# Performance work log

Hardware: AMD Instinct MI355X
Metric: run time of the kernel (lower is better)

## Reference

```python
import jax, jax.numpy as jnp
import numpy as np

GAMMA = 2.0

def setup_inputs() -> dict:
    key = jax.random.key(0)
    k1, k2, k3, k4 = jax.random.split(key, 4)
    B, N, D, C = 4, 512, 128, 10
    x = jax.random.normal(k1, (B, N, D), dtype=jnp.float32)
    span = jax.random.randint(k2, (B, N, N), 0, C, dtype=jnp.int32)
    seqlen = jax.random.randint(k3, (B,), 1, N + 1, dtype=jnp.int32)
    W = jax.random.truncated_normal(k4, -2.0, 2.0, (D, C), dtype=jnp.float32) * 0.02
    b = jnp.zeros((C,), dtype=jnp.float32)
    return {"x": x, "span": span, "seqlen": seqlen, "W": W, "b": b}

def reference(x, span, seqlen, W, b):
    B, N, D = x.shape
    # pairwise tile-multiply: xx[b,i,j,d] = x[b,i,d] * x[b,j,d]
    xx = x[:, :, None, :] * x[:, None, :, :]            # [B,N,N,D]
    logits = jnp.einsum('bijd,dc->bijc', xx, W) + b     # [B,N,N,C]
    sm = jax.nn.softmax(logits, axis=-1)
    # focal loss: gather prob of true class
    prob = jnp.take_along_axis(sm, span[..., None].astype(jnp.int32), axis=-1)[..., 0]
    loss_map = -jnp.power(1.0 - prob, GAMMA) * jnp.log(prob)  # [B,N,N]
    predict = jnp.argmax(sm, axis=-1).astype(jnp.int32)
    # sequence mask [B,N] -> pairwise [B,N,N]
    row = jnp.arange(N)[None, :] < seqlen[:, None]       # [B,N] bool
    val = row[:, None, :] & row[:, :, None]              # [B,N,N]
    valf = val.astype(jnp.float32)
    seqlen2sum = jnp.sum(jnp.square(seqlen.astype(jnp.float32)))
    loss = jnp.sum(loss_map * valf) / seqlen2sum
    predict = predict * val.astype(jnp.int32)
    accuracy = jnp.sum((predict == span).astype(jnp.float32) * valf) / seqlen2sum
    tp = jnp.sum(((predict == span) & (span > 0)).astype(jnp.float32))
    tn = jnp.sum(((predict != span) & (span > 0)).astype(jnp.float32))
    fp = jnp.sum(((predict > 0) & (span <= 0) & val).astype(jnp.float32))
    return (predict, tp, tn, fp, loss, accuracy)
```

## Files before the change

### kernel.cpp

```cpp
#include <hip/hip_runtime.h>
#include <math.h>

#define NB 4
#define NN 512
#define ND 128
#define NC 10
#define NT 32
#define MREP 2
#define NBLK_M (NB*NT*4)

typedef short    bf16x8 __attribute__((ext_vector_type(8)));
typedef unsigned u32x4  __attribute__((ext_vector_type(4)));
typedef float    f32x4  __attribute__((ext_vector_type(4)));

static __device__ __forceinline__ unsigned pack_trunc(float a, float b) {
    unsigned ua = __builtin_bit_cast(unsigned, a);
    unsigned ub = __builtin_bit_cast(unsigned, b);
    return (ua >> 16) | (ub & 0xFFFF0000u);
}

__global__ __launch_bounds__(256) void w2ner_fused(
    const float* __restrict__ x, const int* __restrict__ span,
    const int* __restrict__ seqlen, const float* __restrict__ Wm,
    const float* __restrict__ bias, float* __restrict__ out,
    float* __restrict__ accum)
{
    __shared__ float sRed[4 * 5];
    const int tid = threadIdx.x;
    const int blk = blockIdx.x;
    const int q  = blk & 3;
    const int Tj = (blk >> 2) & 31;
    const int b  = blk >> 7;
    const int wv = tid >> 6, l = tid & 63;
    const int jl = l & 15, kg = l >> 4;
    const int Ti0 = q * 8 + wv * MREP;
    const int j  = Tj * 16 + jl;
    const int sl = seqlen[b];
    const float* xb = x + (size_t)b * NN * ND;

    int sp[MREP][4];
    #pragma unroll
    for (int m = 0; m < MREP; ++m) {
        const int ib = (Ti0 + m) * 16 + kg * 4;
        #pragma unroll
        for (int r = 0; r < 4; ++r)
            sp[m][r] = span[(size_t)b * NN * NN + (size_t)(ib + r) * NN + j];
    }

    f32x4 acc[MREP][NC];
    #pragma unroll
    for (int m = 0; m < MREP; ++m)
        #pragma unroll
        for (int c = 0; c < NC; ++c) acc[m][c] = (f32x4){0.f, 0.f, 0.f, 0.f};

    #pragma unroll
    for (int g = 0; g < 4; ++g) {
        const int d0 = 32 * g + 8 * kg;

        float xj[8];
        *(float4*)&xj[0] = *(const float4*)(xb + (size_t)j * ND + d0);
        *(float4*)&xj[4] = *(const float4*)(xb + (size_t)j * ND + d0 + 4);

        u32x4 ahw[MREP], alw[MREP];
        #pragma unroll
        for (int m = 0; m < MREP; ++m) {
            const int irow = (Ti0 + m) * 16 + jl;
            float xi[8];
            *(float4*)&xi[0] = *(const float4*)(xb + (size_t)irow * ND + d0);
            *(float4*)&xi[4] = *(const float4*)(xb + (size_t)irow * ND + d0 + 4);
            #pragma unroll
            for (int e2 = 0; e2 < 4; ++e2) {
                const float a0 = xi[2 * e2], a1 = xi[2 * e2 + 1];
                const unsigned u0 = __builtin_bit_cast(unsigned, a0) & 0xFFFF0000u;
                const unsigned u1 = __builtin_bit_cast(unsigned, a1) & 0xFFFF0000u;
                const float h0 = __builtin_bit_cast(float, u0);
                const float h1 = __builtin_bit_cast(float, u1);
                ahw[m][e2] = (u0 >> 16) | u1;
                alw[m][e2] = pack_trunc(a0 - h0, a1 - h1);
            }
        }

        u32x4 yw[NC];
        #pragma unroll
        for (int e2 = 0; e2 < 4; ++e2) {
            float wb[20];
            const float4* wp = (const float4*)(Wm + (size_t)(d0 + 2 * e2) * NC);
            #pragma unroll
            for (int t5 = 0; t5 < 5; ++t5) *(float4*)&wb[4 * t5] = wp[t5];
            const float x0 = xj[2 * e2], x1 = xj[2 * e2 + 1];
            #pragma unroll
            for (int c = 0; c < NC; ++c)
                yw[c][e2] = pack_trunc(x0 * wb[c], x1 * wb[10 + c]);
        }

        #pragma unroll
        for (int c = 0; c < NC; ++c) {
            const bf16x8 bh = __builtin_bit_cast(bf16x8, yw[c]);
            #pragma unroll
            for (int m = 0; m < MREP; ++m) {
                const bf16x8 ah = __builtin_bit_cast(bf16x8, ahw[m]);
                const bf16x8 al = __builtin_bit_cast(bf16x8, alw[m]);
                acc[m][c] = __builtin_amdgcn_mfma_f32_16x16x32_bf16(ah, bh, acc[m][c], 0, 0, 0);
                acc[m][c] = __builtin_amdgcn_mfma_f32_16x16x32_bf16(al, bh, acc[m][c], 0, 0, 0);
            }
        }
    }

    float lsum = 0.f, accn = 0.f, tpn = 0.f, tnn = 0.f, fpn = 0.f;
    #pragma unroll
    for (int m = 0; m < MREP; ++m) {
        const int ib = (Ti0 + m) * 16 + kg * 4;
        #pragma unroll
        for (int r = 0; r < 4; ++r) {
            const int i = ib + r;
            float L[NC];
            #pragma unroll
            for (int c = 0; c < NC; ++c) L[c] = acc[m][c][r] + bias[c];
            int am = 0; float mx = L[0];
            #pragma unroll
            for (int c = 1; c < NC; ++c) { if (L[c] > mx) { mx = L[c]; am = c; } }
            float e[NC]; float s = 0.f;
            #pragma unroll
            for (int c = 0; c < NC; ++c) { e[c] = __expf(L[c] - mx); s += e[c]; }
            const int spv = sp[m][r];
            float lsp = L[0], esp = e[0];
            #pragma unroll
            for (int c = 1; c < NC; ++c) {
                lsp = (spv == c) ? L[c] : lsp;
                esp = (spv == c) ? e[c] : esp;
            }
            const float inv  = __builtin_amdgcn_rcpf(s);
            const float lp   = (lsp - mx) - __logf(s);
            const float prob = esp * inv;
            const float om   = 1.f - prob;
            const float lm   = -(om * om) * lp;
            const bool v = (i < sl) && (j < sl);
            const int pred = v ? am : 0;
            out[(size_t)b * NN * NN + (size_t)i * NN + j] = (float)pred;
            if (v) { lsum += lm; if (pred == spv) accn += 1.f; }
            if (spv > 0) { if (pred == spv) tpn += 1.f; else tnn += 1.f; }
            else if (pred > 0 && v) fpn += 1.f;
        }
    }

    float vals[5] = { lsum, accn, tpn, tnn, fpn };
    #pragma unroll
    for (int k = 0; k < 5; ++k) {
        float vv = vals[k];
        for (int o = 32; o > 0; o >>= 1) vv += __shfl_down(vv, o);
        vals[k] = vv;
    }
    if (l == 0) {
        #pragma unroll
        for (int k = 0; k < 5; ++k) sRed[wv * 5 + k] = vals[k];
    }
    __syncthreads();
    if (tid < 5) {
        float t = sRed[tid] + sRed[5 + tid] + sRed[10 + tid] + sRed[15 + tid];
        accum[(size_t)blk * 5 + tid] = t;
    }
}

__global__ __launch_bounds__(256) void w2ner_final(
    const int* __restrict__ seqlen, const float* __restrict__ accum,
    float* __restrict__ out)
{
    __shared__ float sP[4][5];
    const int tid = threadIdx.x;
    float part[5] = {0.f, 0.f, 0.f, 0.f, 0.f};
    for (int r = tid; r < NBLK_M; r += 256) {
        #pragma unroll
        for (int k = 0; k < 5; ++k) part[k] += accum[(size_t)r * 5 + k];
    }
    #pragma unroll
    for (int k = 0; k < 5; ++k) {
        float v = part[k];
        for (int o = 32; o > 0; o >>= 1) v += __shfl_down(v, o);
        part[k] = v;
    }
    const int wave = tid >> 6;
    const int lane = tid & 63;
    if (lane == 0) {
        #pragma unroll
        for (int k = 0; k < 5; ++k) sP[wave][k] = part[k];
    }
    __syncthreads();
    if (tid == 0) {
        float t[5];
        #pragma unroll
        for (int k = 0; k < 5; ++k) t[k] = sP[0][k] + sP[1][k] + sP[2][k] + sP[3][k];
        float s2 = 0.f;
        for (int k = 0; k < NB; ++k) { float s = (float)seqlen[k]; s2 += s * s; }
        const size_t base = (size_t)NB * NN * NN;
        out[base + 0] = t[2];
        out[base + 1] = t[3];
        out[base + 2] = t[4];
        out[base + 3] = t[0] / s2;
        out[base + 4] = t[1] / s2;
    }
}

extern "C" void kernel_launch(void* const* d_in, const int* in_sizes, int n_in,
                              void* d_out, int out_size, void* d_ws, size_t ws_size,
                              hipStream_t stream) {
    const float* x      = (const float*)d_in[0];
    const int*   span   = (const int*)d_in[1];
    const int*   seqlen = (const int*)d_in[2];
    const float* Wm     = (const float*)d_in[3];
    const float* bias   = (const float*)d_in[4];
    float* out   = (float*)d_out;
    float* accum = (float*)d_ws;

    w2ner_fused<<<dim3(NBLK_M), 256, 0, stream>>>(x, span, seqlen, Wm, bias, out, accum);
    w2ner_final<<<1, 256, 0, stream>>>(seqlen, accum, out);
}
```

Baseline: 23.72 us.

## Split work across twice as many blocks, hoist loads, swizzle block order

Each wave now handles a single 16-row i tile instead of two, which doubles the grid to 1024 blocks. All x loads for the i and j rows are hoisted ahead of the MFMA loop so their latency overlaps, and the span loads are issued afterwards. The block index is remapped so that consecutive hardware block IDs are strided across eight groups, apparently to spread work across XCDs and improve L2 locality. The cost is that the W-scaled y operands are recomputed per single tile rather than reused across two, and more blocks write partial sums.

```diff
diff --git a/kernel.cpp b/kernel.cpp
--- a/kernel.cpp
+++ b/kernel.cpp
@@ -6,8 +6,7 @@
 #define ND 128
 #define NC 10
 #define NT 32
-#define MREP 2
-#define NBLK_M (NB*NT*4)
+#define NBLK_M (NB*NT*8)
 
 typedef short    bf16x8 __attribute__((ext_vector_type(8)));
 typedef unsigned u32x4  __attribute__((ext_vector_type(4)));
@@ -27,57 +26,51 @@
 {
     __shared__ float sRed[4 * 5];
     const int tid = threadIdx.x;
-    const int blk = blockIdx.x;
-    const int q  = blk & 3;
-    const int Tj = (blk >> 2) & 31;
-    const int b  = blk >> 7;
+    const int lb = (blockIdx.x & 7) * (NBLK_M / 8) + (blockIdx.x >> 3);
+    const int q  = lb & 7;
+    const int Tj = (lb >> 3) & 31;
+    const int b  = lb >> 8;
     const int wv = tid >> 6, l = tid & 63;
     const int jl = l & 15, kg = l >> 4;
-    const int Ti0 = q * 8 + wv * MREP;
+    const int Ti = q * 4 + wv;
     const int j  = Tj * 16 + jl;
     const int sl = seqlen[b];
     const float* xb = x + (size_t)b * NN * ND;
-
-    int sp[MREP][4];
-    #pragma unroll
-    for (int m = 0; m < MREP; ++m) {
-        const int ib = (Ti0 + m) * 16 + kg * 4;
-        #pragma unroll
-        for (int r = 0; r < 4; ++r)
-            sp[m][r] = span[(size_t)b * NN * NN + (size_t)(ib + r) * NN + j];
-    }
-
-    f32x4 acc[MREP][NC];
-    #pragma unroll
-    for (int m = 0; m < MREP; ++m)
-        #pragma unroll
-        for (int c = 0; c < NC; ++c) acc[m][c] = (f32x4){0.f, 0.f, 0.f, 0.f};
-
+    const int irow = Ti * 16 + jl;
+
+    float xi[4][8], xj[4][8];
     #pragma unroll
     for (int g = 0; g < 4; ++g) {
         const int d0 = 32 * g + 8 * kg;
-
-        float xj[8];
-        *(float4*)&xj[0] = *(const float4*)(xb + (size_t)j * ND + d0);
-        *(float4*)&xj[4] = *(const float4*)(xb + (size_t)j * ND + d0 + 4);
-
-        u32x4 ahw[MREP], alw[MREP];
-        #pragma unroll
-        for (int m = 0; m < MREP; ++m) {
-            const int irow = (Ti0 + m) * 16 + jl;
-            float xi[8];
-            *(float4*)&xi[0] = *(const float4*)(xb + (size_t)irow * ND + d0);
-            *(float4*)&xi[4] = *(const float4*)(xb + (size_t)irow * ND + d0 + 4);
-            #pragma unroll
-            for (int e2 = 0; e2 < 4; ++e2) {
-                const float a0 = xi[2 * e2], a1 = xi[2 * e2 + 1];
-                const unsigned u0 = __builtin_bit_cast(unsigned, a0) & 0xFFFF0000u;
-                const unsigned u1 = __builtin_bit_cast(unsigned, a1) & 0xFFFF0000u;
-                const float h0 = __builtin_bit_cast(float, u0);
-                const float h1 = __builtin_bit_cast(float, u1);
-                ahw[m][e2] = (u0 >> 16) | u1;
-                alw[m][e2] = pack_trunc(a0 - h0, a1 - h1);
-            }
+        *(float4*)&xi[g][0] = *(const float4*)(xb + (size_t)irow * ND + d0);
+        *(float4*)&xi[g][4] = *(const float4*)(xb + (size_t)irow * ND + d0 + 4);
+        *(float4*)&xj[g][0] = *(const float4*)(xb + (size_t)j * ND + d0);
+        *(float4*)&xj[g][4] = *(const float4*)(xb + (size_t)j * ND + d0 + 4);
+    }
+    const int ib = Ti * 16 + kg * 4;
+    int sp[4];
+    #pragma unroll
+    for (int r = 0; r < 4; ++r)
+        sp[r] = span[(size_t)b * NN * NN + (size_t)(ib + r) * NN + j];
+
+    f32x4 acc[NC];
+    #pragma unroll
+    for (int c = 0; c < NC; ++c) acc[c] = (f32x4){0.f, 0.f, 0.f, 0.f};
+
+    #pragma unroll
+    for (int g = 0; g < 4; ++g) {
+        const int d0 = 32 * g + 8 * kg;
+
+        u32x4 ahw, alw;
+        #pragma unroll
+        for (int e2 = 0; e2 < 4; ++e2) {
+            const float a0 = xi[g][2 * e2], a1 = xi[g][2 * e2 + 1];
+            const unsigned u0 = __builtin_bit_cast(unsigned, a0) & 0xFFFF0000u;
+            const unsigned u1 = __builtin_bit_cast(unsigned, a1) & 0xFFFF0000u;
+            const float h0 = __builtin_bit_cast(float, u0);
+            const float h1 = __builtin_bit_cast(float, u1);
+            ahw[e2] = (u0 >> 16) | u1;
+            alw[e2] = pack_trunc(a0 - h0, a1 - h1);
         }
 
         u32x4 yw[NC];
@@ -87,60 +80,53 @@
             const float4* wp = (const float4*)(Wm + (size_t)(d0 + 2 * e2) * NC);
             #pragma unroll
             for (int t5 = 0; t5 < 5; ++t5) *(float4*)&wb[4 * t5] = wp[t5];
-            const float x0 = xj[2 * e2], x1 = xj[2 * e2 + 1];
+            const float x0 = xj[g][2 * e2], x1 = xj[g][2 * e2 + 1];
             #pragma unroll
             for (int c = 0; c < NC; ++c)
                 yw[c][e2] = pack_trunc(x0 * wb[c], x1 * wb[10 + c]);
         }
 
+        const bf16x8 ah = __builtin_bit_cast(bf16x8, ahw);
+        const bf16x8 al = __builtin_bit_cast(bf16x8, alw);
         #pragma unroll
         for (int c = 0; c < NC; ++c) {
             const bf16x8 bh = __builtin_bit_cast(bf16x8, yw[c]);
-            #pragma unroll
-            for (int m = 0; m < MREP; ++m) {
-                const bf16x8 ah = __builtin_bit_cast(bf16x8, ahw[m]);
-                const bf16x8 al = __builtin_bit_cast(bf16x8, alw[m]);
-                acc[m][c] = __builtin_amdgcn_mfma_f32_16x16x32_bf16(ah, bh, acc[m][c], 0, 0, 0);
-                acc[m][c] = __builtin_amdgcn_mfma_f32_16x16x32_bf16(al, bh, acc[m][c], 0, 0, 0);
-            }
+            acc[c] = __builtin_amdgcn_mfma_f32_16x16x32_bf16(ah, bh, acc[c], 0, 0, 0);
+            acc[c] = __builtin_amdgcn_mfma_f32_16x16x32_bf16(al, bh, acc[c], 0, 0, 0);
         }
     }
 
     float lsum = 0.f, accn = 0.f, tpn = 0.f, tnn = 0.f, fpn = 0.f;
     #pragma unroll
-    for (int m = 0; m < MREP; ++m) {
-        const int ib = (Ti0 + m) * 16 + kg * 4;
-        #pragma unroll
-        for (int r = 0; r < 4; ++r) {
-            const int i = ib + r;
-            float L[NC];
-            #pragma unroll
-            for (int c = 0; c < NC; ++c) L[c] = acc[m][c][r] + bias[c];
-            int am = 0; float mx = L[0];
-            #pragma unroll
-            for (int c = 1; c < NC; ++c) { if (L[c] > mx) { mx = L[c]; am = c; } }
-            float e[NC]; float s = 0.f;
-            #pragma unroll
-            for (int c = 0; c < NC; ++c) { e[c] = __expf(L[c] - mx); s += e[c]; }
-            const int spv = sp[m][r];
-            float lsp = L[0], esp = e[0];
-            #pragma unroll
-            for (int c = 1; c < NC; ++c) {
-                lsp = (spv == c) ? L[c] : lsp;
-                esp = (spv == c) ? e[c] : esp;
-            }
-            const float inv  = __builtin_amdgcn_rcpf(s);
-            const float lp   = (lsp - mx) - __logf(s);
-            const float prob = esp * inv;
-            const float om   = 1.f - prob;
-            const float lm   = -(om * om) * lp;
-            const bool v = (i < sl) && (j < sl);
-            const int pred = v ? am : 0;
-            out[(size_t)b * NN * NN + (size_t)i * NN + j] = (float)pred;
-            if (v) { lsum += lm; if (pred == spv) accn += 1.f; }
-            if (spv > 0) { if (pred == spv) tpn += 1.f; else tnn += 1.f; }
-            else if (pred > 0 && v) fpn += 1.f;
-        }
+    for (int r = 0; r < 4; ++r) {
+        const int i = ib + r;
+        float L[NC];
+        #pragma unroll
+        for (int c = 0; c < NC; ++c) L[c] = acc[c][r] + bias[c];
+        int am = 0; float mx = L[0];
+        #pragma unroll
+        for (int c = 1; c < NC; ++c) { if (L[c] > mx) { mx = L[c]; am = c; } }
+        float e[NC]; float s = 0.f;
+        #pragma unroll
+        for (int c = 0; c < NC; ++c) { e[c] = __expf(L[c] - mx); s += e[c]; }
+        const int spv = sp[r];
+        float lsp = L[0], esp = e[0];
+        #pragma unroll
+        for (int c = 1; c < NC; ++c) {
+            lsp = (spv == c) ? L[c] : lsp;
+            esp = (spv == c) ? e[c] : esp;
+        }
+        const float inv  = __builtin_amdgcn_rcpf(s);
+        const float lp   = (lsp - mx) - __logf(s);
+        const float prob = esp * inv;
+        const float om   = 1.f - prob;
+        const float lm   = -(om * om) * lp;
+        const bool v = (i < sl) && (j < sl);
+        const int pred = v ? am : 0;
+        out[(size_t)b * NN * NN + (size_t)i * NN + j] = (float)pred;
+        if (v) { lsum += lm; if (pred == spv) accn += 1.f; }
+        if (spv > 0) { if (pred == spv) tpn += 1.f; else tnn += 1.f; }
+        else if (pred > 0 && v) fpn += 1.f;
     }
 
     float vals[5] = { lsum, accn, tpn, tnn, fpn };
@@ -157,7 +143,7 @@
     __syncthreads();
     if (tid < 5) {
         float t = sRed[tid] + sRed[5 + tid] + sRed[10 + tid] + sRed[15 + tid];
-        accum[(size_t)blk * 5 + tid] = t;
+        accum[(size_t)blockIdx.x * 5 + tid] = t;
     }
 }
 
```

Measured after the change: 31.16 us. +31.4%, slower.
